# Kernel tuning notes

Hardware: AMD Instinct MI355X
Metric: run time of the kernel (lower is better)

Reference implementation:

```python
import jax, jax.numpy as jnp
import numpy as np
import math

D_MODEL = 1024
D_INNER = 2048
D_HALF = D_INNER // 2
D_STATE = 16
D_CONV = 4
DT_RANK = 64
B_SZ = 4
L = 2048


def _dw_conv(x, w, b):
    # x: (b, l, c), w: (k, 1, c) depthwise, SAME padding
    y = jax.lax.conv_general_dilated(
        x, w, window_strides=(1,), padding='SAME',
        feature_group_count=x.shape[-1],
        dimension_numbers=('NWC', 'WIO', 'NWC'))
    return y + b


def _selective_scan(u, delta, A, Bc, Cc, D):
    # u, delta: (b, l, d); Bc, Cc: (b, l, n); A: (d, n); D: (d,)
    b, l, d = u.shape
    n = A.shape[1]

    def step(h, inp):
        d_t, u_t, B_t, C_t = inp  # (b,d), (b,d), (b,n), (b,n)
        dA = jnp.exp(d_t[..., None] * A)                     # (b,d,n)
        h = dA * h + (d_t * u_t)[..., None] * B_t[:, None, :]
        y = jnp.einsum('bdn,bn->bd', h, C_t)
        return h, y

    h0 = jnp.zeros((b, d, n), u.dtype)
    xs = (jnp.moveaxis(delta, 1, 0), jnp.moveaxis(u, 1, 0),
          jnp.moveaxis(Bc, 1, 0), jnp.moveaxis(Cc, 1, 0))
    _, ys = jax.lax.scan(step, h0, xs)                       # (l,b,d)
    return jnp.moveaxis(ys, 0, 1) + u * D


def setup_inputs() -> dict:
    key = jax.random.key(0)
    ks = jax.random.split(key, 12)
    x = jax.random.normal(ks[0], (B_SZ, L, D_MODEL), jnp.float32)
    W_in = jax.random.normal(ks[1], (D_MODEL, D_INNER), jnp.float32) * (D_MODEL ** -0.5)
    conv_x_w = jax.random.normal(ks[2], (D_CONV, 1, D_HALF), jnp.float32) * (D_CONV ** -0.5)
    conv_x_b = jnp.zeros((D_HALF,), jnp.float32)
    conv_z_w = jax.random.normal(ks[3], (D_CONV, 1, D_HALF), jnp.float32) * (D_CONV ** -0.5)
    conv_z_b = jnp.zeros((D_HALF,), jnp.float32)
    W_xdbl = jax.random.normal(ks[4], (D_HALF, DT_RANK + 2 * D_STATE), jnp.float32) * (D_HALF ** -0.5)
    dt_init_std = DT_RANK ** -0.5  # dt_scale = 1.0
    W_dt = jax.random.uniform(ks[5], (DT_RANK, D_HALF), jnp.float32, -dt_init_std, dt_init_std)
    rand_vals = jax.random.uniform(ks[6], (D_HALF,))
    dt_bias = jnp.exp(rand_vals * (math.log(0.1) - math.log(0.001)) + math.log(0.001))
    dt_bias = jnp.clip(dt_bias, 1e-4)
    inv_dt = dt_bias + jnp.log(-jnp.expm1(-dt_bias))
    D = jnp.ones((D_HALF,), jnp.float32)
    W_out = jax.random.normal(ks[7], (D_INNER, D_MODEL), jnp.float32) * (D_INNER ** -0.5)
    b_out = jnp.zeros((D_MODEL,), jnp.float32)
    return dict(x=x, W_in=W_in, conv_x_w=conv_x_w, conv_x_b=conv_x_b,
                conv_z_w=conv_z_w, conv_z_b=conv_z_b, W_xdbl=W_xdbl,
                W_dt=W_dt, inv_dt=inv_dt, D=D, W_out=W_out, b_out=b_out)


def reference(x, W_in, conv_x_w, conv_x_b, conv_z_w, conv_z_b, W_xdbl,
              W_dt, inv_dt, D, W_out, b_out):
    xz = x @ W_in                                            # (b,l,d_inner), no bias
    xs, z = jnp.split(xz, 2, axis=-1)                        # (b,l,d_half) each
    # A = -exp(log(arange(1..N))) tiled over channels
    A = -jnp.tile(jnp.arange(1, D_STATE + 1, dtype=jnp.float32), (D_HALF, 1))  # (d,n)
    xs = jax.nn.silu(_dw_conv(xs, conv_x_w, conv_x_b))
    z = jax.nn.silu(_dw_conv(z, conv_z_w, conv_z_b))
    x_dbl = xs @ W_xdbl                                      # (b,l,dt_rank+2n)
    dt_low, Bc, Cc = jnp.split(x_dbl, [DT_RANK, DT_RANK + D_STATE], axis=-1)
    dt = dt_low @ W_dt + inv_dt                              # Dense with bias_init=inv_dt
    delta = jax.nn.softplus(dt + inv_dt)                     # scan adds delta_bias=inv_dt again (faithful)
    y = _selective_scan(xs, delta, A, Bc, Cc, D)             # (b,l,d_half)
    y = jnp.concatenate([y, z], axis=-1)                     # (b,l,d_inner)
    return y @ W_out + b_out
```

## Files before the change

kernel.cpp:

```cpp
#include <hip/hip_runtime.h>
#include <hip/hip_bf16.h>
#include <math.h>

#define B_SZ 4
#define LSEQ 2048
#define DM 1024
#define DI 2048
#define DH 1024
#define DS 16
#define DTR 64
#define RTOT 96
#define MROWS (B_SZ * LSEQ)

#define NCH 32
#define CHUNK 64

typedef short bf8_t __attribute__((ext_vector_type(8)));
typedef float f4_t __attribute__((ext_vector_type(4)));

__device__ __forceinline__ unsigned short f2bfbits(float v) {
  __hip_bfloat16 h = __float2bfloat16(v);
  return *(unsigned short*)&h;
}
__device__ __forceinline__ float bfu_lo(unsigned int v) {
  unsigned int x = v << 16;
  return *(float*)&x;
}
__device__ __forceinline__ float bfu_hi(unsigned int v) {
  unsigned int x = v & 0xffff0000u;
  return *(float*)&x;
}

__device__ __forceinline__ void gl_lds16(const void* g, void* l) {
  __builtin_amdgcn_global_load_lds(
      (const __attribute__((address_space(1))) unsigned int*)g,
      (__attribute__((address_space(3))) unsigned int*)l,
      16, 0, 0);
}

__device__ __forceinline__ void ld8f(const float* p, unsigned short* d) {
  const float4 a = ((const float4*)p)[0];
  const float4 b = ((const float4*)p)[1];
  d[0] = f2bfbits(a.x); d[1] = f2bfbits(a.y); d[2] = f2bfbits(a.z); d[3] = f2bfbits(a.w);
  d[4] = f2bfbits(b.x); d[5] = f2bfbits(b.y); d[6] = f2bfbits(b.z); d[7] = f2bfbits(b.w);
}

__global__ void probe_kernel(const unsigned short* __restrict__ p, int* __restrict__ flag) {
  int lane = threadIdx.x;
  int sane = 0;
#pragma unroll
  for (int j = 0; j < 4; j++) {
    unsigned short lo = p[(lane * 4 + j) * 2];
    int e = (lo >> 7) & 0xFF;
    sane += (e <= 130) ? 1 : 0;
  }
  sane += __shfl_xor(sane, 1, 64);
  sane += __shfl_xor(sane, 2, 64);
  sane += __shfl_xor(sane, 4, 64);
  sane += __shfl_xor(sane, 8, 64);
  sane += __shfl_xor(sane, 16, 64);
  sane += __shfl_xor(sane, 32, 64);
  if (lane == 0) *flag = (sane >= 220) ? 1 : 0;
}

#define PREP_TOT 78848
__global__ __launch_bounds__(256) void prep_kernel(
    const int* __restrict__ flag,
    const void* s0, const void* s1, const void* s2, const void* s3,
    const void* s4, const void* s5, const void* s6, const void* s7,
    float* __restrict__ out) {
  int i = blockIdx.x * 256 + threadIdx.x;
  if (i >= PREP_TOT) return;
  const void* src; int off;
  if      (i < 4096)   { src = s0; off = i; }
  else if (i < 5120)   { src = s1; off = i - 4096; }
  else if (i < 9216)   { src = s2; off = i - 5120; }
  else if (i < 10240)  { src = s3; off = i - 9216; }
  else if (i < 75776)  { src = s4; off = i - 10240; }
  else if (i < 76800)  { src = s5; off = i - 75776; }
  else if (i < 77824)  { src = s6; off = i - 76800; }
  else                 { src = s7; off = i - 77824; }
  float v = (*flag == 1) ? __bfloat162float(((const __hip_bfloat16*)src)[off])
                         : ((const float*)src)[off];
  out[i] = v;
}

__global__ __launch_bounds__(256) void transpose_kernel(
    const int* __restrict__ flag, const void* __restrict__ W,
    unsigned short* __restrict__ Wt, int K, int N) {
  __shared__ unsigned short tile[32][33];
  int n0 = blockIdx.x * 32, k0 = blockIdx.y * 32;
  int c = threadIdx.x & 31, r8 = threadIdx.x >> 5;
  bool isbf = (*flag == 1);
#pragma unroll
  for (int p = 0; p < 4; p++) {
    int r = r8 + p * 8;
    unsigned short v;
    if (isbf) v = ((const unsigned short*)W)[(size_t)(k0 + r) * N + n0 + c];
    else      v = f2bfbits(((const float*)W)[(size_t)(k0 + r) * N + n0 + c]);
    tile[r][c] = v;
  }
  __syncthreads();
#pragma unroll
  for (int p = 0; p < 4; p++) {
    int r = r8 + p * 8;
    Wt[(size_t)(n0 + r) * K + k0 + c] = tile[c][r];
  }
}

__global__ __launch_bounds__(256) void transpose_pad_kernel(
    const int* __restrict__ flag, const void* __restrict__ W,
    unsigned short* __restrict__ Wt) {
  __shared__ unsigned short tile[32][33];
  int n0 = blockIdx.x * 32, k0 = blockIdx.y * 32;
  int c = threadIdx.x & 31, r8 = threadIdx.x >> 5;
  bool isbf = (*flag == 1);
#pragma unroll
  for (int p = 0; p < 4; p++) {
    int r = r8 + p * 8;
    unsigned short v = 0;
    if (n0 + c < RTOT) {
      if (isbf) v = ((const unsigned short*)W)[(size_t)(k0 + r) * RTOT + n0 + c];
      else      v = f2bfbits(((const float*)W)[(size_t)(k0 + r) * RTOT + n0 + c]);
    }
    tile[r][c] = v;
  }
  __syncthreads();
#pragma unroll
  for (int p = 0; p < 4; p++) {
    int r = r8 + p * 8;
    Wt[(size_t)(n0 + r) * DH + k0 + c] = tile[c][r];
  }
}

template <int BN, bool A_BF, bool O_BF>
__global__ __launch_bounds__(512, 2) void gemm256_tpl(
    const int* __restrict__ flag, int want,
    const void* __restrict__ A, const unsigned short* __restrict__ Bt,
    const float* __restrict__ bias, void* __restrict__ C,
    int M, int N, int K) {
  if (*flag != want) return;
  extern __shared__ __align__(16) unsigned short lds[];
  constexpr int A_TILE = 256 * 64;
  constexpr int B_TILE = BN * 64;
  constexpr int NF = BN / 64;

  const int tid = threadIdx.x;
  const int lane = tid & 63;
  const int wave = tid >> 6;
  const int quad = lane >> 4;
  const int l16 = lane & 15;
  const int wm = wave >> 2;
  const int wn = wave & 3;

  const int NB = gridDim.x, MB = gridDim.y;
  int L = blockIdx.y * NB + blockIdx.x;
  int xcd = L & 7;
  int w = L >> 3;
  int m_band = xcd * (MB >> 3) + (w / NB);
  int n_blk = w % NB;
  const int m0 = m_band * 256;
  const int n0 = n_blk * BN;

  f4_t acc[8][NF] = {};

  auto stage = [&](int k0, int b) {
    unsigned short* Ad = lds + b * A_TILE;
#pragma unroll
    for (int j = 0; j < 4; j++) {
      int ch = tid + j * 512;
      int mi = ch >> 3, s = ch & 7;
      int ki = s ^ (mi & 7);
      if (A_BF) {
        gl_lds16((const unsigned short*)A + (size_t)(m0 + mi) * K + k0 + ki * 8,
                 Ad + (j * 512 + wave * 64) * 8);
      } else {
        unsigned short tmp[8];
        ld8f((const float*)A + (size_t)(m0 + mi) * K + k0 + ki * 8, tmp);
        *(uint4*)&Ad[ch * 8] = *(uint4*)tmp;
      }
    }
    unsigned short* Bd = lds + 2 * A_TILE + b * B_TILE;
#pragma unroll
    for (int j = 0; j < NF; j++) {
      int ch = tid + j * 512;
      int ni = ch >> 3, s = ch & 7;
      int ki = s ^ (ni & 7);
      gl_lds16(Bt + (size_t)(n0 + ni) * K + k0 + ki * 8,
               Bd + (j * 512 + wave * 64) * 8);
    }
  };

  stage(0, 0);
  __syncthreads();
  int cur = 0;
  for (int k0 = 0; k0 < K; k0 += 64) {
    if (k0 + 64 < K) stage(k0 + 64, cur ^ 1);

    const unsigned short* Ac = lds + cur * A_TILE;
    const unsigned short* Bc = lds + 2 * A_TILE + cur * B_TILE;
#pragma unroll
    for (int h = 0; h < 2; h++) {
      bf8_t af[8], bfr[NF];
#pragma unroll
      for (int ti = 0; ti < 8; ti++) {
        int r = wm * 128 + ti * 16 + l16;
        af[ti] = *(const bf8_t*)&Ac[(r * 8 + ((h * 4 + quad) ^ (r & 7))) * 8];
      }
#pragma unroll
      for (int tj = 0; tj < NF; tj++) {
        int rn = wn * (BN / 4) + tj * 16 + l16;
        bfr[tj] = *(const bf8_t*)&Bc[(rn * 8 + ((h * 4 + quad) ^ (rn & 7))) * 8];
      }
      __builtin_amdgcn_s_setprio(1);
#pragma unroll
      for (int ti = 0; ti < 8; ti++)
#pragma unroll
        for (int tj = 0; tj < NF; tj++)
          acc[ti][tj] = __builtin_amdgcn_mfma_f32_16x16x32_bf16(
              af[ti], bfr[tj], acc[ti][tj], 0, 0, 0);
      __builtin_amdgcn_s_setprio(0);
    }
    __syncthreads();
    cur ^= 1;
  }

#pragma unroll
  for (int ti = 0; ti < 8; ti++) {
#pragma unroll
    for (int tj = 0; tj < NF; tj++) {
      int col = n0 + wn * (BN / 4) + tj * 16 + l16;
      float bv = bias ? bias[col] : 0.f;
#pragma unroll
      for (int r = 0; r < 4; r++) {
        int row = m0 + wm * 128 + ti * 16 + quad * 4 + r;
        float v = acc[ti][tj][r] + bv;
        if (O_BF) ((__hip_bfloat16*)C)[(size_t)row * N + col] = __float2bfloat16(v);
        else      ((float*)C)[(size_t)row * N + col] = v;
      }
    }
  }
}

__global__ __launch_bounds__(256) void xdbl_mfma_kernel(
    const unsigned short* __restrict__ A, const unsigned short* __restrict__ Bt,
    float* __restrict__ xdbl) {
  __shared__ __align__(16) unsigned short As[64 * 32];
  __shared__ __align__(16) unsigned short Bs[128 * 32];
  const int tid = threadIdx.x;
  const int lane = tid & 63;
  const int wave = tid >> 6;
  const int quad = lane >> 4;
  const int l16 = lane & 15;
  const int m0 = blockIdx.x * 64;

  f4_t acc[6] = {};

  for (int k0 = 0; k0 < DH; k0 += 32) {
    {
      int ch = tid;
      int mi = ch >> 2;
      int ki = (ch & 3) ^ ((mi >> 1) & 3);
      gl_lds16(A + (size_t)(m0 + mi) * DH + k0 + ki * 8, &As[(wave * 64) * 8]);
    }
#pragma unroll
    for (int j = 0; j < 2; j++) {
      int ch = tid + j * 256;
      int ni = ch >> 2;
      int ki = (ch & 3) ^ ((ni >> 1) & 3);
      gl_lds16(Bt + (size_t)ni * DH + k0 + ki * 8, &Bs[(j * 256 + wave * 64) * 8]);
    }
    __syncthreads();

    bf8_t af, bfr[6];
    {
      int r = wave * 16 + l16;
      af = *(const bf8_t*)&As[(r * 4 + (quad ^ ((r >> 1) & 3))) * 8];
    }
#pragma unroll
    for (int tj = 0; tj < 6; tj++) {
      int r = tj * 16 + l16;
      bfr[tj] = *(const bf8_t*)&Bs[(r * 4 + (quad ^ ((r >> 1) & 3))) * 8];
    }
#pragma unroll
    for (int tj = 0; tj < 6; tj++)
      acc[tj] = __builtin_amdgcn_mfma_f32_16x16x32_bf16(af, bfr[tj], acc[tj], 0, 0, 0);
    __syncthreads();
  }

#pragma unroll
  for (int tj = 0; tj < 6; tj++) {
    int col = tj * 16 + l16;
#pragma unroll
    for (int r = 0; r < 4; r++) {
      int row = m0 + wave * 16 + quad * 4 + r;
      xdbl[(size_t)row * RTOT + col] = acc[tj][r];
    }
  }
}

__global__ __launch_bounds__(256) void conv_silu_kernel(
    const unsigned short* __restrict__ xz,
    const float* __restrict__ wx, const float* __restrict__ bx,
    const float* __restrict__ wz, const float* __restrict__ bz,
    unsigned short* __restrict__ xs_bf, unsigned short* __restrict__ cat) {
  int gid = blockIdx.x * 256 + threadIdx.x;
  int cg = gid & 127;
  int c0 = cg * 8;
  int m = gid >> 7;
  int t = m & (LSEQ - 1);
  float ax[8], az[8];
#pragma unroll
  for (int i = 0; i < 8; i++) { ax[i] = bx[c0 + i]; az[i] = bz[c0 + i]; }
#pragma unroll
  for (int j = 0; j < 4; j++) {
    int tt = t - 1 + j;
    if (tt < 0 || tt >= LSEQ) continue;
    size_t row = (size_t)(m - t + tt);
    uint4 vx = *(const uint4*)&xz[row * DI + c0];
    uint4 vz = *(const uint4*)&xz[row * DI + DH + c0];
    const unsigned int* px = (const unsigned int*)&vx;
    const unsigned int* pz = (const unsigned int*)&vz;
#pragma unroll
    for (int q = 0; q < 4; q++) {
      float x0 = bfu_lo(px[q]), x1 = bfu_hi(px[q]);
      float z0 = bfu_lo(pz[q]), z1 = bfu_hi(pz[q]);
      ax[q * 2]     = fmaf(wx[j * DH + c0 + q * 2], x0, ax[q * 2]);
      ax[q * 2 + 1] = fmaf(wx[j * DH + c0 + q * 2 + 1], x1, ax[q * 2 + 1]);
      az[q * 2]     = fmaf(wz[j * DH + c0 + q * 2], z0, az[q * 2]);
      az[q * 2 + 1] = fmaf(wz[j * DH + c0 + q * 2 + 1], z1, az[q * 2 + 1]);
    }
  }
  unsigned short sx[8], sz[8];
#pragma unroll
  for (int i = 0; i < 8; i++) {
    float vx = ax[i] / (1.f + __expf(-ax[i]));
    float vz = az[i] / (1.f + __expf(-az[i]));
    sx[i] = f2bfbits(vx);
    sz[i] = f2bfbits(vz);
  }
  *(uint4*)&xs_bf[(size_t)m * DH + c0] = *(uint4*)sx;
  *(uint4*)&cat[(size_t)m * DI + DH + c0] = *(uint4*)sz;
}

__global__ __launch_bounds__(256) void delta_kernel(
    const float* __restrict__ xdbl, const float* __restrict__ Wdt,
    const float* __restrict__ inv_dt, const unsigned short* __restrict__ xs,
    unsigned int* __restrict__ du) {
  const int d = blockIdx.x * 256 + threadIdx.x;
  const int m0 = blockIdx.y * 8;
  __shared__ float xr[8][DTR];
#pragma unroll
  for (int i = 0; i < 2; i++) {
    int e = threadIdx.x + i * 256;
    xr[e >> 6][e & 63] = xdbl[(size_t)(m0 + (e >> 6)) * RTOT + (e & 63)];
  }
  __syncthreads();
  float acc[8];
#pragma unroll
  for (int i = 0; i < 8; i++) acc[i] = 0.f;
  for (int rr = 0; rr < DTR; rr++) {
    float w = Wdt[(size_t)rr * DH + d];
#pragma unroll
    for (int i = 0; i < 8; i++) acc[i] = fmaf(xr[i][rr], w, acc[i]);
  }
  const float bias2 = 2.f * inv_dt[d];
#pragma unroll
  for (int i = 0; i < 8; i++) {
    float v = acc[i] + bias2;
    float sp = (v > 0.f) ? (v + log1pf(__expf(-v))) : log1pf(__expf(v));
    unsigned int lo = f2bfbits(sp);
    unsigned int hi = xs[(size_t)(m0 + i) * DH + d];
    du[(size_t)(m0 + i) * DH + d] = lo | (hi << 16);
  }
}

__global__ __launch_bounds__(256) void scan_pass1(
    const unsigned int* __restrict__ du, const float* __restrict__ xdbl,
    float* __restrict__ Echunks, float* __restrict__ hp) {
  const int tid = threadIdx.x;
  const int d = blockIdx.x * 256 + tid;
  const int c = blockIdx.y, b = blockIdx.z;
  const int row0 = b * LSEQ + c * CHUNK;
  __shared__ float sBC[CHUNK][32];
#pragma unroll
  for (int i = 0; i < 2; i++) {
    int task = tid + i * 256;
    int r = task >> 3, seg = task & 7;
    *(float4*)&sBC[r][seg * 4] =
        *(const float4*)&xdbl[(size_t)(row0 + r) * RTOT + DTR + seg * 4];
  }
  __syncthreads();
  float h[16];
#pragma unroll
  for (int n = 0; n < 16; n++) h[n] = 0.f;
  float E = 1.f;
  for (int t = 0; t < CHUNK; t++) {
    unsigned int v = du[(size_t)(row0 + t) * DH + d];
    float dt = bfu_lo(v), ut = bfu_hi(v);
    float e = __expf(-dt);
    E *= e;
    float dv = dt * ut;
    float p = 1.f;
#pragma unroll
    for (int n = 0; n < 16; n++) {
      p *= e;
      h[n] = fmaf(p, h[n], dv * sBC[t][n]);
    }
  }
  Echunks[((size_t)c * B_SZ + b) * DH + d] = E;
#pragma unroll
  for (int n = 0; n < 16; n++)
    hp[(((size_t)c * B_SZ + b) * 16 + n) * DH + d] = h[n];
}

__global__ __launch_bounds__(256) void scan_pass2(
    const float* __restrict__ Echunks, const float* __restrict__ hp,
    float* __restrict__ hs) {
  int t = blockIdx.x * 256 + threadIdx.x;
  int d = t & 1023;
  int n = (t >> 10) & 15;
  int b = t >> 14;
  float h = 0.f;
  const int k0 = n + 1;
  for (int c = 0; c < NCH; c++) {
    float E = Echunks[((size_t)c * B_SZ + b) * DH + d];
    float a = 1.f, base = E;
    int k = k0;
#pragma unroll
    for (int i = 0; i < 5; i++) {
      if (k & 1) a *= base;
      base *= base;
      k >>= 1;
    }
    size_t idx = (((size_t)c * B_SZ + b) * 16 + n) * DH + d;
    hs[idx] = h;
    h = fmaf(a, h, hp[idx]);
  }
}

__global__ __launch_bounds__(256) void scan_pass3(
    const unsigned int* __restrict__ du, const float* __restrict__ xdbl,
    const float* __restrict__ hs, const float* __restrict__ Dvec,
    __hip_bfloat16* __restrict__ cat) {
  const int tid = threadIdx.x;
  const int d = blockIdx.x * 256 + tid;
  const int c = blockIdx.y, b = blockIdx.z;
  const int row0 = b * LSEQ + c * CHUNK;
  __shared__ float sBC[CHUNK][32];
#pragma unroll
  for (int i = 0; i < 2; i++) {
    int task = tid + i * 256;
    int r = task >> 3, seg = task & 7;
    *(float4*)&sBC[r][seg * 4] =
        *(const float4*)&xdbl[(size_t)(row0 + r) * RTOT + DTR + seg * 4];
  }
  __syncthreads();
  float h[16];
#pragma unroll
  for (int n = 0; n < 16; n++)
    h[n] = hs[(((size_t)c * B_SZ + b) * 16 + n) * DH + d];
  const float Dd = Dvec[d];
  for (int t = 0; t < CHUNK; t++) {
    unsigned int v = du[(size_t)(row0 + t) * DH + d];
    float dt = bfu_lo(v), ut = bfu_hi(v);
    float e = __expf(-dt);
    float dv = dt * ut;
    float p = 1.f, y = 0.f;
#pragma unroll
    for (int n = 0; n < 16; n++) {
      p *= e;
      h[n] = fmaf(p, h[n], dv * sBC[t][n]);
      y = fmaf(h[n], sBC[t][16 + n], y);
    }
    y = fmaf(ut, Dd, y);
    cat[(size_t)(row0 + t) * DI + d] = __float2bfloat16(y);
  }
}

extern "C" void kernel_launch(void* const* d_in, const int* in_sizes, int n_in,
                              void* d_out, int out_size, void* d_ws, size_t ws_size,
                              hipStream_t stream) {
  char* ws = (char*)d_ws;
  __hip_bfloat16* xz  = (__hip_bfloat16*)(ws);
  unsigned int* du    = (unsigned int*)(ws);
  __hip_bfloat16* xs  = (__hip_bfloat16*)(ws + ((size_t)32 << 20));
  __hip_bfloat16* cat = (__hip_bfloat16*)(ws + ((size_t)64 << 20));
  float* xdbl         = (float*)(ws + ((size_t)96 << 20));
  float* Echunks      = (float*)(ws + ((size_t)99 << 20));
  float* hp           = (float*)(ws + ((size_t)100 << 20));
  float* hs           = (float*)(ws + ((size_t)108 << 20));
  unsigned short* Wt_in  = (unsigned short*)(ws + ((size_t)116 << 20));
  unsigned short* Wt_out = (unsigned short*)(ws + ((size_t)120 << 20));
  unsigned short* Wxt    = (unsigned short*)(ws + ((size_t)124 << 20));
  float* cw           = (float*)(ws + ((size_t)125 << 20));
  int* flag           = (int*)(ws + ((size_t)126 << 20));

  const float* conv_xwf = cw + 0;
  const float* conv_xbf = cw + 4096;
  const float* conv_zwf = cw + 5120;
  const float* conv_zbf = cw + 9216;
  const float* Wdtf     = cw + 10240;
  const float* inv_dtf  = cw + 75776;
  const float* Df       = cw + 76800;
  const float* b_outf   = cw + 77824;

  (void)hipFuncSetAttribute(reinterpret_cast<const void*>(&gemm256_tpl<256, true, true>),
                            hipFuncAttributeMaxDynamicSharedMemorySize, 131072);
  (void)hipFuncSetAttribute(reinterpret_cast<const void*>(&gemm256_tpl<256, false, true>),
                            hipFuncAttributeMaxDynamicSharedMemorySize, 131072);
  (void)hipFuncSetAttribute(reinterpret_cast<const void*>(&gemm256_tpl<128, true, true>),
                            hipFuncAttributeMaxDynamicSharedMemorySize, 98304);
  (void)hipFuncSetAttribute(reinterpret_cast<const void*>(&gemm256_tpl<128, true, false>),
                            hipFuncAttributeMaxDynamicSharedMemorySize, 98304);

  probe_kernel<<<1, 64, 0, stream>>>((const unsigned short*)d_in[0], flag);
  prep_kernel<<<(PREP_TOT + 255) / 256, 256, 0, stream>>>(
      flag, d_in[2], d_in[3], d_in[4], d_in[5], d_in[7], d_in[8], d_in[9],
      d_in[11], cw);
  transpose_kernel<<<dim3(DI / 32, DM / 32), 256, 0, stream>>>(
      flag, d_in[1], Wt_in, DM, DI);
  transpose_kernel<<<dim3(DM / 32, DI / 32), 256, 0, stream>>>(
      flag, d_in[10], Wt_out, DI, DM);
  transpose_pad_kernel<<<dim3(4, DH / 32), 256, 0, stream>>>(flag, d_in[6], Wxt);

  gemm256_tpl<256, true, true><<<dim3(DI / 256, MROWS / 256), 512, 131072, stream>>>(
      flag, 1, d_in[0], Wt_in, (const float*)nullptr, xz, MROWS, DI, DM);
  gemm256_tpl<256, false, true><<<dim3(DI / 256, MROWS / 256), 512, 131072, stream>>>(
      flag, 0, d_in[0], Wt_in, (const float*)nullptr, xz, MROWS, DI, DM);
  conv_silu_kernel<<<(MROWS * 128) / 256, 256, 0, stream>>>(
      (const unsigned short*)xz, conv_xwf, conv_xbf, conv_zwf, conv_zbf,
      (unsigned short*)xs, (unsigned short*)cat);
  xdbl_mfma_kernel<<<MROWS / 64, 256, 0, stream>>>(
      (const unsigned short*)xs, Wxt, xdbl);
  delta_kernel<<<dim3(4, MROWS / 8), 256, 0, stream>>>(
      xdbl, Wdtf, inv_dtf, (const unsigned short*)xs, du);
  scan_pass1<<<dim3(4, NCH, B_SZ), 256, 0, stream>>>(du, xdbl, Echunks, hp);
  scan_pass2<<<256, 256, 0, stream>>>(Echunks, hp, hs);
  scan_pass3<<<dim3(4, NCH, B_SZ), 256, 0, stream>>>(du, xdbl, hs, Df, cat);
  gemm256_tpl<128, true, true><<<dim3(DM / 128, MROWS / 256), 512, 98304, stream>>>(
      flag, 1, cat, Wt_out, b_outf, d_out, MROWS, DM, DI);
  gemm256_tpl<128, true, false><<<dim3(DM / 128, MROWS / 256), 512, 98304, stream>>>(
      flag, 0, cat, Wt_out, b_outf, d_out, MROWS, DM, DI);
}
```

Measured before the change: 373.5 us.

## Rewrite GEMMs with 4-stage BK32 pipeline, pre-cast input, direct-load xdbl kernel

Result: no change. 375.2 us (+0.4%).

```diff
diff --git a/kernel.cpp b/kernel.cpp
--- a/kernel.cpp
+++ b/kernel.cpp
@@ -37,6 +37,12 @@
       (__attribute__((address_space(3))) unsigned int*)l,
       16, 0, 0);
 }
+__device__ __forceinline__ void gl_lds16_nt(const void* g, void* l) {
+  __builtin_amdgcn_global_load_lds(
+      (const __attribute__((address_space(1))) unsigned int*)g,
+      (__attribute__((address_space(3))) unsigned int*)l,
+      16, 0, 2);
+}
 
 __device__ __forceinline__ void ld8f(const float* p, unsigned short* d) {
   const float4 a = ((const float4*)p)[0];
@@ -44,6 +50,9 @@
   d[0] = f2bfbits(a.x); d[1] = f2bfbits(a.y); d[2] = f2bfbits(a.z); d[3] = f2bfbits(a.w);
   d[4] = f2bfbits(b.x); d[5] = f2bfbits(b.y); d[6] = f2bfbits(b.z); d[7] = f2bfbits(b.w);
 }
+
+#define VMCNT(n) asm volatile("s_waitcnt vmcnt(" #n ")" ::: "memory")
+#define LGKM0 asm volatile("s_waitcnt lgkmcnt(0)" ::: "memory")
 
 __global__ void probe_kernel(const unsigned short* __restrict__ p, int* __restrict__ flag) {
   int lane = threadIdx.x;
@@ -61,6 +70,16 @@
   sane += __shfl_xor(sane, 16, 64);
   sane += __shfl_xor(sane, 32, 64);
   if (lane == 0) *flag = (sane >= 220) ? 1 : 0;
+}
+
+__global__ __launch_bounds__(256) void cast_kernel(
+    const int* __restrict__ flag, const float* __restrict__ x,
+    unsigned short* __restrict__ xbf) {
+  if (*flag == 1) return;
+  int i = (blockIdx.x * 256 + threadIdx.x) * 8;
+  unsigned short d[8];
+  ld8f(x + i, d);
+  *(uint4*)&xbf[i] = *(uint4*)d;
 }
 
 #define PREP_TOT 78848
@@ -133,17 +152,22 @@
   }
 }
 
-template <int BN, bool A_BF, bool O_BF>
-__global__ __launch_bounds__(512, 2) void gemm256_tpl(
-    const int* __restrict__ flag, int want,
-    const void* __restrict__ A, const unsigned short* __restrict__ Bt,
+template <int BN, bool OUT_BY_FLAG>
+__global__ __launch_bounds__(512, 2) void gemm_bk32(
+    const int* __restrict__ flag,
+    const unsigned short* __restrict__ A1, const unsigned short* __restrict__ A0,
+    const unsigned short* __restrict__ Bt,
     const float* __restrict__ bias, void* __restrict__ C,
-    int M, int N, int K) {
-  if (*flag != want) return;
+    int N, int K) {
   extern __shared__ __align__(16) unsigned short lds[];
-  constexpr int A_TILE = 256 * 64;
-  constexpr int B_TILE = BN * 64;
+  constexpr int A_BUF = 256 * 32;
+  constexpr int B_BUF = BN * 32;
+  constexpr int B_OFF = 4 * A_BUF;
   constexpr int NF = BN / 64;
+  constexpr int NB_LD = BN / 128;
+
+  const int flagv = *flag;
+  const unsigned short* Ap = (flagv == 1) ? A1 : A0;
 
   const int tid = threadIdx.x;
   const int lane = tid & 63;
@@ -162,67 +186,71 @@
   const int m0 = m_band * 256;
   const int n0 = n_blk * BN;
 
+  const int NT = K >> 5;
+
   f4_t acc[8][NF] = {};
 
-  auto stage = [&](int k0, int b) {
-    unsigned short* Ad = lds + b * A_TILE;
-#pragma unroll
-    for (int j = 0; j < 4; j++) {
+  auto stage = [&](int kt) {
+    const int buf = kt & 3;
+    const int k0 = kt * 32;
+    unsigned short* Ad = lds + buf * A_BUF;
+#pragma unroll
+    for (int j = 0; j < 2; j++) {
       int ch = tid + j * 512;
-      int mi = ch >> 3, s = ch & 7;
-      int ki = s ^ (mi & 7);
-      if (A_BF) {
-        gl_lds16((const unsigned short*)A + (size_t)(m0 + mi) * K + k0 + ki * 8,
-                 Ad + (j * 512 + wave * 64) * 8);
-      } else {
-        unsigned short tmp[8];
-        ld8f((const float*)A + (size_t)(m0 + mi) * K + k0 + ki * 8, tmp);
-        *(uint4*)&Ad[ch * 8] = *(uint4*)tmp;
-      }
-    }
-    unsigned short* Bd = lds + 2 * A_TILE + b * B_TILE;
-#pragma unroll
-    for (int j = 0; j < NF; j++) {
+      int mi = ch >> 2, s = ch & 3;
+      int ki = s ^ ((mi >> 1) & 3);
+      gl_lds16_nt(Ap + (size_t)(m0 + mi) * K + k0 + ki * 8,
+                  Ad + (j * 512 + wave * 64) * 8);
+    }
+    unsigned short* Bd = lds + B_OFF + buf * B_BUF;
+#pragma unroll
+    for (int j = 0; j < NB_LD; j++) {
       int ch = tid + j * 512;
-      int ni = ch >> 3, s = ch & 7;
-      int ki = s ^ (ni & 7);
+      int ni = ch >> 2, s = ch & 3;
+      int ki = s ^ ((ni >> 1) & 3);
       gl_lds16(Bt + (size_t)(n0 + ni) * K + k0 + ki * 8,
                Bd + (j * 512 + wave * 64) * 8);
     }
   };
 
-  stage(0, 0);
-  __syncthreads();
-  int cur = 0;
-  for (int k0 = 0; k0 < K; k0 += 64) {
-    if (k0 + 64 < K) stage(k0 + 64, cur ^ 1);
-
-    const unsigned short* Ac = lds + cur * A_TILE;
-    const unsigned short* Bc = lds + 2 * A_TILE + cur * B_TILE;
-#pragma unroll
-    for (int h = 0; h < 2; h++) {
-      bf8_t af[8], bfr[NF];
-#pragma unroll
-      for (int ti = 0; ti < 8; ti++) {
-        int r = wm * 128 + ti * 16 + l16;
-        af[ti] = *(const bf8_t*)&Ac[(r * 8 + ((h * 4 + quad) ^ (r & 7))) * 8];
-      }
-#pragma unroll
-      for (int tj = 0; tj < NF; tj++) {
-        int rn = wn * (BN / 4) + tj * 16 + l16;
-        bfr[tj] = *(const bf8_t*)&Bc[(rn * 8 + ((h * 4 + quad) ^ (rn & 7))) * 8];
-      }
-      __builtin_amdgcn_s_setprio(1);
-#pragma unroll
-      for (int ti = 0; ti < 8; ti++)
-#pragma unroll
-        for (int tj = 0; tj < NF; tj++)
-          acc[ti][tj] = __builtin_amdgcn_mfma_f32_16x16x32_bf16(
-              af[ti], bfr[tj], acc[ti][tj], 0, 0, 0);
-      __builtin_amdgcn_s_setprio(0);
-    }
-    __syncthreads();
-    cur ^= 1;
+  stage(0); stage(1); stage(2);
+
+  for (int t = 0; t < NT; t++) {
+    if (t + 2 < NT) {
+      if constexpr (NF == 4) VMCNT(8); else VMCNT(6);
+    } else if (t + 1 < NT) {
+      if constexpr (NF == 4) VMCNT(4); else VMCNT(3);
+    } else {
+      VMCNT(0);
+    }
+    __builtin_amdgcn_s_barrier();
+
+    const unsigned short* Ac = lds + (t & 3) * A_BUF;
+    const unsigned short* Bc = lds + B_OFF + (t & 3) * B_BUF;
+    bf8_t af[8], bfr[NF];
+#pragma unroll
+    for (int ti = 0; ti < 8; ti++) {
+      int r = wm * 128 + ti * 16 + l16;
+      af[ti] = *(const bf8_t*)&Ac[(r * 4 + (quad ^ ((r >> 1) & 3))) * 8];
+    }
+#pragma unroll
+    for (int tj = 0; tj < NF; tj++) {
+      int rn = wn * (BN / 4) + tj * 16 + l16;
+      bfr[tj] = *(const bf8_t*)&Bc[(rn * 4 + (quad ^ ((rn >> 1) & 3))) * 8];
+    }
+    if (t + 3 < NT) stage(t + 3);
+
+    LGKM0;
+    __builtin_amdgcn_sched_barrier(0);
+    __builtin_amdgcn_s_setprio(1);
+#pragma unroll
+    for (int ti = 0; ti < 8; ti++)
+#pragma unroll
+      for (int tj = 0; tj < NF; tj++)
+        acc[ti][tj] = __builtin_amdgcn_mfma_f32_16x16x32_bf16(
+            af[ti], bfr[tj], acc[ti][tj], 0, 0, 0);
+    __builtin_amdgcn_s_setprio(0);
+    __builtin_amdgcn_s_barrier();
   }
 
 #pragma unroll
@@ -235,65 +263,55 @@
       for (int r = 0; r < 4; r++) {
         int row = m0 + wm * 128 + ti * 16 + quad * 4 + r;
         float v = acc[ti][tj][r] + bv;
-        if (O_BF) ((__hip_bfloat16*)C)[(size_t)row * N + col] = __float2bfloat16(v);
-        else      ((float*)C)[(size_t)row * N + col] = v;
+        if constexpr (!OUT_BY_FLAG) {
+          __builtin_nontemporal_store(f2bfbits(v),
+              (unsigned short*)C + (size_t)row * N + col);
+        } else {
+          if (flagv == 1)
+            __builtin_nontemporal_store(f2bfbits(v),
+                (unsigned short*)C + (size_t)row * N + col);
+          else
+            __builtin_nontemporal_store(v, (float*)C + (size_t)row * N + col);
+        }
       }
     }
   }
 }
 
-__global__ __launch_bounds__(256) void xdbl_mfma_kernel(
+__global__ __launch_bounds__(256) void xdbl_kernel(
     const unsigned short* __restrict__ A, const unsigned short* __restrict__ Bt,
     float* __restrict__ xdbl) {
-  __shared__ __align__(16) unsigned short As[64 * 32];
-  __shared__ __align__(16) unsigned short Bs[128 * 32];
   const int tid = threadIdx.x;
+  const int wave = tid >> 6;
   const int lane = tid & 63;
-  const int wave = tid >> 6;
   const int quad = lane >> 4;
   const int l16 = lane & 15;
-  const int m0 = blockIdx.x * 64;
-
-  f4_t acc[6] = {};
-
+  const int m0 = blockIdx.x * 32 + (wave & 1) * 16;
+  const int c0 = (wave >> 1) * 48;
+
+  f4_t acc[3] = {};
+  const unsigned short* Ar = A + (size_t)(m0 + l16) * DH + quad * 8;
+  const unsigned short* B0 = Bt + (size_t)(c0 + l16) * DH + quad * 8;
+  const unsigned short* B1 = Bt + (size_t)(c0 + 16 + l16) * DH + quad * 8;
+  const unsigned short* B2 = Bt + (size_t)(c0 + 32 + l16) * DH + quad * 8;
+
+#pragma unroll 4
   for (int k0 = 0; k0 < DH; k0 += 32) {
-    {
-      int ch = tid;
-      int mi = ch >> 2;
-      int ki = (ch & 3) ^ ((mi >> 1) & 3);
-      gl_lds16(A + (size_t)(m0 + mi) * DH + k0 + ki * 8, &As[(wave * 64) * 8]);
-    }
-#pragma unroll
-    for (int j = 0; j < 2; j++) {
-      int ch = tid + j * 256;
-      int ni = ch >> 2;
-      int ki = (ch & 3) ^ ((ni >> 1) & 3);
-      gl_lds16(Bt + (size_t)ni * DH + k0 + ki * 8, &Bs[(j * 256 + wave * 64) * 8]);
-    }
-    __syncthreads();
-
-    bf8_t af, bfr[6];
-    {
-      int r = wave * 16 + l16;
-      af = *(const bf8_t*)&As[(r * 4 + (quad ^ ((r >> 1) & 3))) * 8];
-    }
-#pragma unroll
-    for (int tj = 0; tj < 6; tj++) {
-      int r = tj * 16 + l16;
-      bfr[tj] = *(const bf8_t*)&Bs[(r * 4 + (quad ^ ((r >> 1) & 3))) * 8];
-    }
-#pragma unroll
-    for (int tj = 0; tj < 6; tj++)
-      acc[tj] = __builtin_amdgcn_mfma_f32_16x16x32_bf16(af, bfr[tj], acc[tj], 0, 0, 0);
-    __syncthreads();
-  }
-
-#pragma unroll
-  for (int tj = 0; tj < 6; tj++) {
-    int col = tj * 16 + l16;
+    bf8_t af = *(const bf8_t*)(Ar + k0);
+    bf8_t b0 = *(const bf8_t*)(B0 + k0);
+    bf8_t b1 = *(const bf8_t*)(B1 + k0);
+    bf8_t b2 = *(const bf8_t*)(B2 + k0);
+    acc[0] = __builtin_amdgcn_mfma_f32_16x16x32_bf16(af, b0, acc[0], 0, 0, 0);
+    acc[1] = __builtin_amdgcn_mfma_f32_16x16x32_bf16(af, b1, acc[1], 0, 0, 0);
+    acc[2] = __builtin_amdgcn_mfma_f32_16x16x32_bf16(af, b2, acc[2], 0, 0, 0);
+  }
+
+#pragma unroll
+  for (int tj = 0; tj < 3; tj++) {
+    int col = c0 + tj * 16 + l16;
 #pragma unroll
     for (int r = 0; r < 4; r++) {
-      int row = m0 + wave * 16 + quad * 4 + r;
+      int row = m0 + quad * 4 + r;
       xdbl[(size_t)row * RTOT + col] = acc[tj][r];
     }
   }
@@ -485,6 +503,7 @@
   __hip_bfloat16* xz  = (__hip_bfloat16*)(ws);
   unsigned int* du    = (unsigned int*)(ws);
   __hip_bfloat16* xs  = (__hip_bfloat16*)(ws + ((size_t)32 << 20));
+  unsigned short* xbf = (unsigned short*)(ws + ((size_t)48 << 20));
   __hip_bfloat16* cat = (__hip_bfloat16*)(ws + ((size_t)64 << 20));
   float* xdbl         = (float*)(ws + ((size_t)96 << 20));
   float* Echunks      = (float*)(ws + ((size_t)99 << 20));
@@ -505,16 +524,13 @@
   const float* Df       = cw + 76800;
   const float* b_outf   = cw + 77824;
 
-  (void)hipFuncSetAttribute(reinterpret_cast<const void*>(&gemm256_tpl<256, true, true>),
+  (void)hipFuncSetAttribute(reinterpret_cast<const void*>(&gemm_bk32<256, false>),
                             hipFuncAttributeMaxDynamicSharedMemorySize, 131072);
-  (void)hipFuncSetAttribute(reinterpret_cast<const void*>(&gemm256_tpl<256, false, true>),
-                            hipFuncAttributeMaxDynamicSharedMemorySize, 131072);
-  (void)hipFuncSetAttribute(reinterpret_cast<const void*>(&gemm256_tpl<128, true, true>),
+  (void)hipFuncSetAttribute(reinterpret_cast<const void*>(&gemm_bk32<128, true>),
                             hipFuncAttributeMaxDynamicSharedMemorySize, 98304);
-  (void)hipFuncSetAttribute(reinterpret_cast<const void*>(&gemm256_tpl<128, true, false>),
-                            hipFuncAttributeMaxDynamicSharedMemorySize, 98304);
 
   probe_kernel<<<1, 64, 0, stream>>>((const unsigned short*)d_in[0], flag);
+  cast_kernel<<<4096, 256, 0, stream>>>(flag, (const float*)d_in[0], xbf);
   prep_kernel<<<(PREP_TOT + 255) / 256, 256, 0, stream>>>(
       flag, d_in[2], d_in[3], d_in[4], d_in[5], d_in[7], d_in[8], d_in[9],
       d_in[11], cw);
@@ -524,22 +540,20 @@
       flag, d_in[10], Wt_out, DI, DM);
   transpose_pad_kernel<<<dim3(4, DH / 32), 256, 0, stream>>>(flag, d_in[6], Wxt);
 
-  gemm256_tpl<256, true, true><<<dim3(DI / 256, MROWS / 256), 512, 131072, stream>>>(
-      flag, 1, d_in[0], Wt_in, (const float*)nullptr, xz, MROWS, DI, DM);
-  gemm256_tpl<256, false, true><<<dim3(DI / 256, MROWS / 256), 512, 131072, stream>>>(
-      flag, 0, d_in[0], Wt_in, (const float*)nullptr, xz, MROWS, DI, DM);
+  gemm_bk32<256, false><<<dim3(DI / 256, MROWS / 256), 512, 131072, stream>>>(
+      flag, (const unsigned short*)d_in[0], xbf, Wt_in,
+      (const float*)nullptr, xz, DI, DM);
   conv_silu_kernel<<<(MROWS * 128) / 256, 256, 0, stream>>>(
       (const unsigned short*)xz, conv_xwf, conv_xbf, conv_zwf, conv_zbf,
       (unsigned short*)xs, (unsigned short*)cat);
-  xdbl_mfma_kernel<<<MROWS / 64, 256, 0, stream>>>(
+  xdbl_kernel<<<MROWS / 32, 256, 0, stream>>>(
       (const unsigned short*)xs, Wxt, xdbl);
   delta_kernel<<<dim3(4, MROWS / 8), 256, 0, stream>>>(
       xdbl, Wdtf, inv_dtf, (const unsigned short*)xs, du);
   scan_pass1<<<dim3(4, NCH, B_SZ), 256, 0, stream>>>(du, xdbl, Echunks, hp);
   scan_pass2<<<256, 256, 0, stream>>>(Echunks, hp, hs);
   scan_pass3<<<dim3(4, NCH, B_SZ), 256, 0, stream>>>(du, xdbl, hs, Df, cat);
-  gemm256_tpl<128, true, true><<<dim3(DM / 128, MROWS / 256), 512, 98304, stream>>>(
-      flag, 1, cat, Wt_out, b_outf, d_out, MROWS, DM, DI);
-  gemm256_tpl<128, true, false><<<dim3(DM / 128, MROWS / 256), 512, 98304, stream>>>(
-      flag, 0, cat, Wt_out, b_outf, d_out, MROWS, DM, DI);
-}
+  gemm_bk32<128, true><<<dim3(DM / 128, MROWS / 256), 512, 98304, stream>>>(
+      flag, (const unsigned short*)cat, (const unsigned short*)cat, Wt_out,
+      b_outf, d_out, DM, DI);
+}
```
